# Performance work log

Measured on AMD Instinct MI355X. Metric: run time of the kernel, lower is better.

The kernel has to match this reference:

```python
import jax, jax.numpy as jnp
import numpy as np

N_NODES = 100000
IN_CH = 256
OUT_CH = 128
HEADS = 1
N_EDGES = 1600000
NEG_SLOPE = 0.2
EPS = 1e-16


def setup_inputs() -> dict:
    key = jax.random.key(0)
    ks = jax.random.split(key, 6)
    x = jax.random.normal(ks[0], (N_NODES, IN_CH), dtype=jnp.float32)
    edge_index = jax.random.randint(ks[1], (2, N_EDGES), 0, N_NODES, dtype=jnp.int64)
    # xavier-ish scaled params
    lin_src = jax.random.normal(ks[2], (IN_CH, OUT_CH), dtype=jnp.float32) * (1.414 * (2.0 / (IN_CH + OUT_CH)) ** 0.5)
    att_src = jax.random.normal(ks[3], (1, HEADS, OUT_CH), dtype=jnp.float32) * 0.1
    att_dst = jax.random.normal(ks[4], (1, HEADS, OUT_CH), dtype=jnp.float32) * 0.1
    bias = jnp.zeros((HEADS * OUT_CH,), dtype=jnp.float32)
    return {"x": x, "edge_index": edge_index, "lin_src": lin_src,
            "att_src": att_src, "att_dst": att_dst, "bias": bias}


def reference(x, edge_index, lin_src, att_src, att_dst, bias):
    N = x.shape[0]
    # shared projection (lin_dst is lin_src when in_channels is an int)
    xp = (x @ lin_src).reshape(N, HEADS, OUT_CH)  # [N, H, C]

    # add_self_loops: drop existing self-edges (via mask) and append N loop edges
    src, dst = edge_index[0], edge_index[1]
    loop = jnp.arange(N, dtype=edge_index.dtype)
    src_all = jnp.concatenate([src, loop])
    dst_all = jnp.concatenate([dst, loop])
    valid = jnp.concatenate([src != dst, jnp.ones((N,), dtype=bool)])  # [E+N]

    # per-node attention logits
    alpha_src = jnp.sum(xp * att_src, axis=-1)  # [N, H]
    alpha_dst = jnp.sum(xp * att_dst, axis=-1)  # [N, H]
    alpha = alpha_src[src_all] + alpha_dst[dst_all]  # [E+N, H]
    alpha = jax.nn.leaky_relu(alpha, NEG_SLOPE)

    # scatter softmax over incoming edges of each dst node (global-max stabilized,
    # matching the original src.max() over all retained edges)
    amax = jnp.max(jnp.where(valid[:, None], alpha, -jnp.inf))
    ex = jnp.exp(alpha - amax) * valid[:, None].astype(alpha.dtype)
    denom = jax.ops.segment_sum(ex, dst_all, num_segments=N)  # [N, H]
    alpha = ex / (denom[dst_all] + EPS)  # [E+N, H]

    # weighted aggregation
    weighted = xp[src_all] * alpha[..., None]  # [E+N, H, C]
    out = jax.ops.segment_sum(weighted, dst_all, num_segments=N)  # [N, H, C]

    out = out.reshape(N, HEADS * OUT_CH) + bias  # concat=True
    return out
```

## Files before the change

kernel.cpp:

```cpp
#include <hip/hip_runtime.h>
#include <cstdint>
#include <cstddef>

#define IN_CH 256
#define OUT_CH 128
#define NEG_SLOPE 0.2f
#define EPS 1e-16f

#define BM 64
#define BN 128
#define BK 32

__device__ __forceinline__ void gemm_body(
    int bid,
    const float* __restrict__ x, const float* __restrict__ w,
    const float* __restrict__ att_s, const float* __restrict__ att_d,
    float* __restrict__ xp, float* __restrict__ asrc, float* __restrict__ adst,
    int M)
{
    __shared__ float sA[BK][BM + 4];
    __shared__ float sB[BK][BN];
    const int tid = threadIdx.x;
    const int ty = tid >> 4;
    const int tx = tid & 15;
    const int row0 = bid * BM;

    float acc[4][8];
#pragma unroll
    for (int i = 0; i < 4; ++i)
#pragma unroll
        for (int j = 0; j < 8; ++j) acc[i][j] = 0.f;

    const int ar = tid >> 2;
    const int ak = (tid & 3) * 8;
    const int bk = tid >> 3;
    const int bn = (tid & 7) * 16;

    for (int k0 = 0; k0 < IN_CH; k0 += BK) {
        float4 va0 = make_float4(0.f, 0.f, 0.f, 0.f), va1 = va0;
        const int grow = row0 + ar;
        if (grow < M) {
            const float4* pa = (const float4*)(x + (size_t)grow * IN_CH + k0 + ak);
            va0 = pa[0]; va1 = pa[1];
        }
        sA[ak + 0][ar] = va0.x; sA[ak + 1][ar] = va0.y;
        sA[ak + 2][ar] = va0.z; sA[ak + 3][ar] = va0.w;
        sA[ak + 4][ar] = va1.x; sA[ak + 5][ar] = va1.y;
        sA[ak + 6][ar] = va1.z; sA[ak + 7][ar] = va1.w;

        {
            const float4* pb = (const float4*)(w + (size_t)(k0 + bk) * OUT_CH + bn);
            float4 vb0 = pb[0], vb1 = pb[1], vb2 = pb[2], vb3 = pb[3];
            float4* qb = (float4*)&sB[bk][bn];
            qb[0] = vb0; qb[1] = vb1; qb[2] = vb2; qb[3] = vb3;
        }
        __syncthreads();

#pragma unroll
        for (int k = 0; k < BK; ++k) {
            float4 a4 = *(const float4*)&sA[k][ty * 4];
            float4 b0 = *(const float4*)&sB[k][tx * 8];
            float4 b1 = *(const float4*)&sB[k][tx * 8 + 4];
            float a[4] = { a4.x, a4.y, a4.z, a4.w };
            float b[8] = { b0.x, b0.y, b0.z, b0.w, b1.x, b1.y, b1.z, b1.w };
#pragma unroll
            for (int i = 0; i < 4; ++i)
#pragma unroll
                for (int j = 0; j < 8; ++j)
                    acc[i][j] += a[i] * b[j];
        }
        __syncthreads();
    }

    float as[8], ad[8];
#pragma unroll
    for (int j = 0; j < 8; ++j) {
        as[j] = att_s[tx * 8 + j];
        ad[j] = att_d[tx * 8 + j];
    }
#pragma unroll
    for (int i = 0; i < 4; ++i) {
        const int r = row0 + ty * 4 + i;
        if (r < M) {
            float4 o0 = make_float4(acc[i][0], acc[i][1], acc[i][2], acc[i][3]);
            float4 o1 = make_float4(acc[i][4], acc[i][5], acc[i][6], acc[i][7]);
            float4* q = (float4*)(xp + (size_t)r * OUT_CH + tx * 8);
            q[0] = o0; q[1] = o1;
            float ps = 0.f, pd = 0.f;
#pragma unroll
            for (int j = 0; j < 8; ++j) {
                ps += acc[i][j] * as[j];
                pd += acc[i][j] * ad[j];
            }
#pragma unroll
            for (int m = 8; m >= 1; m >>= 1) {
                ps += __shfl_xor(ps, m, 16);
                pd += __shfl_xor(pd, m, 16);
            }
            if (tx == 0) { asrc[r] = ps; adst[r] = pd; }
        }
    }
}

__device__ __forceinline__ void hist_body(
    int bid, int nblk,
    const int* __restrict__ src, const int* __restrict__ dst,
    int* __restrict__ deg, int* __restrict__ pw, int E)
{
    const int T = nblk * 256;
    const int e0 = bid * 256 + threadIdx.x;
#pragma unroll
    for (int k = 0; k < 4; ++k) {
        const int e = e0 + k * T;
        if (e < E) {
            int s = src[e], d = dst[e];
            if (s != d) pw[e] = atomicAdd(&deg[d], 1);
        }
    }
}

__global__ __launch_bounds__(256) void fused_gemm_hist_kernel(
    const float* __restrict__ x, const float* __restrict__ w,
    const float* __restrict__ att_s, const float* __restrict__ att_d,
    float* __restrict__ xp, float* __restrict__ asrc, float* __restrict__ adst,
    int M,
    const int* __restrict__ src, const int* __restrict__ dst,
    int* __restrict__ deg, int* __restrict__ pw, int E,
    int gemm_blocks, int hist_blocks)
{
    if ((int)blockIdx.x < gemm_blocks) {
        gemm_body(blockIdx.x, x, w, att_s, att_d, xp, asrc, adst, M);
    } else {
        hist_body(blockIdx.x - gemm_blocks, hist_blocks, src, dst, deg, pw, E);
    }
}

#define SCAN_NB 256
#define SCAN_NT 256

__global__ __launch_bounds__(SCAN_NT) void scan_partial_kernel(
    const int* __restrict__ deg, int* __restrict__ bsum, int N)
{
    __shared__ int sh[SCAN_NT];
    const int chunk = (N + SCAN_NB - 1) / SCAN_NB;
    const int sub   = (chunk + SCAN_NT - 1) / SCAN_NT;
    const int b0 = blockIdx.x * chunk;
    const int t0 = b0 + threadIdx.x * sub;
    const int t1 = min(min(b0 + chunk, t0 + sub), N);
    int s = 0;
    for (int i = t0; i < t1; ++i) s += deg[i];
    sh[threadIdx.x] = s;
    __syncthreads();
    for (int off = SCAN_NT / 2; off > 0; off >>= 1) {
        if (threadIdx.x < off) sh[threadIdx.x] += sh[threadIdx.x + off];
        __syncthreads();
    }
    if (threadIdx.x == 0) bsum[blockIdx.x] = sh[0];
}

__global__ __launch_bounds__(SCAN_NB) void scan_blocksums_kernel(
    const int* __restrict__ bsum, int* __restrict__ boff,
    int* __restrict__ row_ptr, int N)
{
    __shared__ int sh[SCAN_NB];
    const int t = threadIdx.x;
    sh[t] = bsum[t];
    __syncthreads();
    for (int off = 1; off < SCAN_NB; off <<= 1) {
        int v = (t >= off) ? sh[t - off] : 0;
        __syncthreads();
        sh[t] += v;
        __syncthreads();
    }
    boff[t] = (t == 0) ? 0 : sh[t - 1];
    if (t == SCAN_NB - 1) row_ptr[N] = sh[t];
}

__global__ __launch_bounds__(SCAN_NT) void scan_fill_kernel(
    const int* __restrict__ deg, const int* __restrict__ boff,
    int* __restrict__ row_ptr, int N)
{
    __shared__ int sh[SCAN_NT];
    const int chunk = (N + SCAN_NB - 1) / SCAN_NB;
    const int sub   = (chunk + SCAN_NT - 1) / SCAN_NT;
    const int b0 = blockIdx.x * chunk;
    const int t0 = b0 + threadIdx.x * sub;
    const int t1 = min(min(b0 + chunk, t0 + sub), N);
    int s = 0;
    for (int i = t0; i < t1; ++i) s += deg[i];
    sh[threadIdx.x] = s;
    __syncthreads();
    for (int off = 1; off < SCAN_NT; off <<= 1) {
        int v = (threadIdx.x >= off) ? sh[threadIdx.x - off] : 0;
        __syncthreads();
        sh[threadIdx.x] += v;
        __syncthreads();
    }
    int run = boff[blockIdx.x] + ((threadIdx.x == 0) ? 0 : sh[threadIdx.x - 1]);
    for (int i = t0; i < t1; ++i) {
        row_ptr[i] = run;
        run += deg[i];
    }
}

__global__ __launch_bounds__(256) void scatter_kernel(
    const int* __restrict__ src, const int* __restrict__ dst,
    const int* __restrict__ row_ptr, const int* __restrict__ pw,
    int* __restrict__ col, int E, int nblk)
{
    const int T = nblk * 256;
    const int e0 = blockIdx.x * 256 + threadIdx.x;
#pragma unroll
    for (int k = 0; k < 4; ++k) {
        const int e = e0 + k * T;
        if (e < E) {
            int s = src[e], d = dst[e];
            if (s != d) col[row_ptr[d] + pw[e]] = s;
        }
    }
}

__global__ __launch_bounds__(256) void aggregate_kernel(
    const float* __restrict__ xp, const float* __restrict__ asrc,
    const float* __restrict__ adst, const int* __restrict__ row_ptr,
    const int* __restrict__ col, const float* __restrict__ bias,
    float* __restrict__ out, int N)
{
    const int wave = (blockIdx.x * blockDim.x + threadIdx.x) >> 6;
    const int lane = threadIdx.x & 63;
    if (wave >= N) return;
    const int n = wave;
    const float a_d = adst[n];

    const float2* xp2 = (const float2*)xp;
    float accx = 0.f, accy = 0.f, denom = 0.f;

    {
        float lg = asrc[n] + a_d;
        lg = (lg > 0.f) ? lg : lg * NEG_SLOPE;
        float ex = __expf(lg);
        denom += ex;
        float2 v = xp2[(size_t)n * 64 + lane];
        accx += ex * v.x; accy += ex * v.y;
    }

    const int beg = row_ptr[n];
    const int end = row_ptr[n + 1];
    for (int base = beg; base < end; base += 64) {
        const int idx = base + lane;
        int s = 0; float ex = 0.f;
        if (idx < end) {
            s = col[idx];
            float lg = asrc[s] + a_d;
            lg = (lg > 0.f) ? lg : lg * NEG_SLOPE;
            ex = __expf(lg);
        }
        const int cnt = min(64, end - base);
        for (int j = 0; j < cnt; ++j) {
            const float exj = __shfl(ex, j, 64);
            const int   sj  = __shfl(s, j, 64);
            denom += exj;
            float2 v = xp2[(size_t)sj * 64 + lane];
            accx += exj * v.x; accy += exj * v.y;
        }
    }

    const float inv = 1.f / (denom + EPS);
    const float2* bias2 = (const float2*)bias;
    float2 bv = bias2[lane];
    float2 o; o.x = accx * inv + bv.x; o.y = accy * inv + bv.y;
    ((float2*)out)[(size_t)n * 64 + lane] = o;
}

extern "C" void kernel_launch(void* const* d_in, const int* in_sizes, int n_in,
                              void* d_out, int out_size, void* d_ws, size_t ws_size,
                              hipStream_t stream)
{
    const float* x     = (const float*)d_in[0];
    const int*   ei    = (const int*)d_in[1];
    const float* w     = (const float*)d_in[2];
    const float* att_s = (const float*)d_in[3];
    const float* att_d = (const float*)d_in[4];
    const float* bias  = (const float*)d_in[5];
    float* out = (float*)d_out;

    const int N = in_sizes[0] / IN_CH;
    const int E = in_sizes[1] / 2;
    const int* src = ei;
    const int* dst = ei + E;

    char* p = (char*)d_ws;
    float* xp      = (float*)p; p += (size_t)N * OUT_CH * sizeof(float);
    float* asrc    = (float*)p; p += (size_t)N * sizeof(float);
    float* adst    = (float*)p; p += (size_t)N * sizeof(float);
    int*   deg     = (int*)p;   p += (size_t)N * sizeof(int);
    int*   row_ptr = (int*)p;   p += (size_t)(N + 1) * sizeof(int);
    int*   bsum    = (int*)p;   p += (size_t)SCAN_NB * sizeof(int);
    int*   boff    = (int*)p;   p += (size_t)SCAN_NB * sizeof(int);
    int*   pw      = (int*)p;   p += (size_t)E * sizeof(int);
    int*   col     = (int*)p;   p += (size_t)E * sizeof(int);

    hipMemsetAsync(deg, 0, (size_t)N * sizeof(int), stream);

    const int gemm_blocks = (N + BM - 1) / BM;
    const int hist_blocks = (E + 256 * 4 - 1) / (256 * 4);
    fused_gemm_hist_kernel<<<gemm_blocks + hist_blocks, 256, 0, stream>>>(
        x, w, att_s, att_d, xp, asrc, adst, N,
        src, dst, deg, pw, E, gemm_blocks, hist_blocks);

    scan_partial_kernel<<<SCAN_NB, SCAN_NT, 0, stream>>>(deg, bsum, N);
    scan_blocksums_kernel<<<1, SCAN_NB, 0, stream>>>(bsum, boff, row_ptr, N);
    scan_fill_kernel<<<SCAN_NB, SCAN_NT, 0, stream>>>(deg, boff, row_ptr, N);

    const int sc_blocks = (E + 256 * 4 - 1) / (256 * 4);
    scatter_kernel<<<sc_blocks, 256, 0, stream>>>(src, dst, row_ptr, pw, col, E, sc_blocks);

    aggregate_kernel<<<(N + 3) / 4, 256, 0, stream>>>(
        xp, asrc, adst, row_ptr, col, bias, out, N);
}
```

Before: 436.9 us.

## Use bf16 MFMA projection, store bf16 features, unroll aggregation gather

Replaces the FP32 SIMT GEMM with bf16 MFMA 16x16x32 instructions, using a pre-transposed bf16 copy of the weights made by a new conversion kernel. The projected features are stored as bf16, which halves the bytes read in the random gather of the aggregation kernel. The aggregation loop is unrolled by four with independent accumulators so more gather loads are in flight at once. Histogram and scatter kernels process eight edges per thread, and hist blocks are ordered before GEMM blocks. Reduced precision in the features and attention logits may loosen accuracy against the reference.

```diff
diff --git a/kernel.cpp b/kernel.cpp
--- a/kernel.cpp
+++ b/kernel.cpp
@@ -7,97 +7,85 @@
 #define NEG_SLOPE 0.2f
 #define EPS 1e-16f
 
-#define BM 64
-#define BN 128
-#define BK 32
+typedef __attribute__((ext_vector_type(8))) short bf16x8;
+typedef __attribute__((ext_vector_type(4))) float f32x4;
+
+__device__ __forceinline__ unsigned short f2bf(float f) {
+    unsigned int u = __float_as_uint(f);
+    return (unsigned short)((u + 0x7fffu + ((u >> 16) & 1u)) >> 16);
+}
+
+__global__ __launch_bounds__(256) void convert_w_kernel(const float* __restrict__ w,
+                                                        unsigned short* __restrict__ wt)
+{
+    const int n = blockIdx.x;
+    const int k = threadIdx.x;
+    wt[(size_t)n * IN_CH + k] = f2bf(w[(size_t)k * OUT_CH + n]);
+}
 
 __device__ __forceinline__ void gemm_body(
-    int bid,
-    const float* __restrict__ x, const float* __restrict__ w,
+    int bid, const float* __restrict__ x, const unsigned short* __restrict__ wt,
     const float* __restrict__ att_s, const float* __restrict__ att_d,
-    float* __restrict__ xp, float* __restrict__ asrc, float* __restrict__ adst,
+    unsigned short* __restrict__ xpb, float* __restrict__ asrc, float* __restrict__ adst,
     int M)
 {
-    __shared__ float sA[BK][BM + 4];
-    __shared__ float sB[BK][BN];
-    const int tid = threadIdx.x;
-    const int ty = tid >> 4;
-    const int tx = tid & 15;
-    const int row0 = bid * BM;
-
-    float acc[4][8];
-#pragma unroll
-    for (int i = 0; i < 4; ++i)
-#pragma unroll
-        for (int j = 0; j < 8; ++j) acc[i][j] = 0.f;
-
-    const int ar = tid >> 2;
-    const int ak = (tid & 3) * 8;
-    const int bk = tid >> 3;
-    const int bn = (tid & 7) * 16;
-
-    for (int k0 = 0; k0 < IN_CH; k0 += BK) {
-        float4 va0 = make_float4(0.f, 0.f, 0.f, 0.f), va1 = va0;
-        const int grow = row0 + ar;
-        if (grow < M) {
-            const float4* pa = (const float4*)(x + (size_t)grow * IN_CH + k0 + ak);
-            va0 = pa[0]; va1 = pa[1];
-        }
-        sA[ak + 0][ar] = va0.x; sA[ak + 1][ar] = va0.y;
-        sA[ak + 2][ar] = va0.z; sA[ak + 3][ar] = va0.w;
-        sA[ak + 4][ar] = va1.x; sA[ak + 5][ar] = va1.y;
-        sA[ak + 6][ar] = va1.z; sA[ak + 7][ar] = va1.w;
-
-        {
-            const float4* pb = (const float4*)(w + (size_t)(k0 + bk) * OUT_CH + bn);
-            float4 vb0 = pb[0], vb1 = pb[1], vb2 = pb[2], vb3 = pb[3];
-            float4* qb = (float4*)&sB[bk][bn];
-            qb[0] = vb0; qb[1] = vb1; qb[2] = vb2; qb[3] = vb3;
-        }
-        __syncthreads();
-
-#pragma unroll
-        for (int k = 0; k < BK; ++k) {
-            float4 a4 = *(const float4*)&sA[k][ty * 4];
-            float4 b0 = *(const float4*)&sB[k][tx * 8];
-            float4 b1 = *(const float4*)&sB[k][tx * 8 + 4];
-            float a[4] = { a4.x, a4.y, a4.z, a4.w };
-            float b[8] = { b0.x, b0.y, b0.z, b0.w, b1.x, b1.y, b1.z, b1.w };
-#pragma unroll
-            for (int i = 0; i < 4; ++i)
-#pragma unroll
-                for (int j = 0; j < 8; ++j)
-                    acc[i][j] += a[i] * b[j];
-        }
-        __syncthreads();
-    }
-
-    float as[8], ad[8];
-#pragma unroll
-    for (int j = 0; j < 8; ++j) {
-        as[j] = att_s[tx * 8 + j];
-        ad[j] = att_d[tx * 8 + j];
-    }
-#pragma unroll
-    for (int i = 0; i < 4; ++i) {
-        const int r = row0 + ty * 4 + i;
-        if (r < M) {
-            float4 o0 = make_float4(acc[i][0], acc[i][1], acc[i][2], acc[i][3]);
-            float4 o1 = make_float4(acc[i][4], acc[i][5], acc[i][6], acc[i][7]);
-            float4* q = (float4*)(xp + (size_t)r * OUT_CH + tx * 8);
-            q[0] = o0; q[1] = o1;
+    const int tid  = threadIdx.x;
+    const int wv   = tid >> 6;
+    const int lane = tid & 63;
+    const int lm   = lane & 15;
+    const int quad = lane >> 4;
+    const int arow = bid * 64 + wv * 16 + lm;
+    const bool av  = arow < M;
+    const float* xrow = x + (size_t)arow * IN_CH + quad * 8;
+
+    f32x4 acc[8];
+#pragma unroll
+    for (int t = 0; t < 8; ++t) acc[t] = (f32x4){0.f, 0.f, 0.f, 0.f};
+
+#pragma unroll
+    for (int kk = 0; kk < 8; ++kk) {
+        const int k0 = kk * 32;
+        bf16x8 af = {0, 0, 0, 0, 0, 0, 0, 0};
+        if (av) {
+            float4 a0 = *(const float4*)(xrow + k0);
+            float4 a1 = *(const float4*)(xrow + k0 + 4);
+            af[0] = (short)f2bf(a0.x); af[1] = (short)f2bf(a0.y);
+            af[2] = (short)f2bf(a0.z); af[3] = (short)f2bf(a0.w);
+            af[4] = (short)f2bf(a1.x); af[5] = (short)f2bf(a1.y);
+            af[6] = (short)f2bf(a1.z); af[7] = (short)f2bf(a1.w);
+        }
+#pragma unroll
+        for (int t = 0; t < 8; ++t) {
+            bf16x8 bf = *(const bf16x8*)(wt + (size_t)(16 * t + lm) * IN_CH + k0 + quad * 8);
+            acc[t] = __builtin_amdgcn_mfma_f32_16x16x32_bf16(af, bf, acc[t], 0, 0, 0);
+        }
+    }
+
+    float asw[8], adw[8];
+#pragma unroll
+    for (int t = 0; t < 8; ++t) {
+        asw[t] = att_s[16 * t + lm];
+        adw[t] = att_d[16 * t + lm];
+    }
+#pragma unroll
+    for (int r = 0; r < 4; ++r) {
+        const int orow = bid * 64 + wv * 16 + quad * 4 + r;
+        if (orow < M) {
             float ps = 0.f, pd = 0.f;
-#pragma unroll
-            for (int j = 0; j < 8; ++j) {
-                ps += acc[i][j] * as[j];
-                pd += acc[i][j] * ad[j];
+            unsigned short* xr = xpb + (size_t)orow * OUT_CH + lm;
+#pragma unroll
+            for (int t = 0; t < 8; ++t) {
+                float v = acc[t][r];
+                xr[16 * t] = f2bf(v);
+                ps += v * asw[t];
+                pd += v * adw[t];
             }
 #pragma unroll
-            for (int m = 8; m >= 1; m >>= 1) {
+            for (int m = 1; m < 16; m <<= 1) {
                 ps += __shfl_xor(ps, m, 16);
                 pd += __shfl_xor(pd, m, 16);
             }
-            if (tx == 0) { asrc[r] = ps; adst[r] = pd; }
+            if (lm == 0) { asrc[orow] = ps; adst[orow] = pd; }
         }
     }
 }
@@ -110,7 +98,7 @@
     const int T = nblk * 256;
     const int e0 = bid * 256 + threadIdx.x;
 #pragma unroll
-    for (int k = 0; k < 4; ++k) {
+    for (int k = 0; k < 8; ++k) {
         const int e = e0 + k * T;
         if (e < E) {
             int s = src[e], d = dst[e];
@@ -120,19 +108,18 @@
 }
 
 __global__ __launch_bounds__(256) void fused_gemm_hist_kernel(
-    const float* __restrict__ x, const float* __restrict__ w,
+    const float* __restrict__ x, const unsigned short* __restrict__ wt,
     const float* __restrict__ att_s, const float* __restrict__ att_d,
-    float* __restrict__ xp, float* __restrict__ asrc, float* __restrict__ adst,
+    unsigned short* __restrict__ xpb, float* __restrict__ asrc, float* __restrict__ adst,
     int M,
     const int* __restrict__ src, const int* __restrict__ dst,
     int* __restrict__ deg, int* __restrict__ pw, int E,
-    int gemm_blocks, int hist_blocks)
-{
-    if ((int)blockIdx.x < gemm_blocks) {
-        gemm_body(blockIdx.x, x, w, att_s, att_d, xp, asrc, adst, M);
-    } else {
-        hist_body(blockIdx.x - gemm_blocks, hist_blocks, src, dst, deg, pw, E);
-    }
+    int hist_blocks)
+{
+    if ((int)blockIdx.x < hist_blocks)
+        hist_body(blockIdx.x, hist_blocks, src, dst, deg, pw, E);
+    else
+        gemm_body(blockIdx.x - hist_blocks, x, wt, att_s, att_d, xpb, asrc, adst, M);
 }
 
 #define SCAN_NB 256
@@ -211,7 +198,7 @@
     const int T = nblk * 256;
     const int e0 = blockIdx.x * 256 + threadIdx.x;
 #pragma unroll
-    for (int k = 0; k < 4; ++k) {
+    for (int k = 0; k < 8; ++k) {
         const int e = e0 + k * T;
         if (e < E) {
             int s = src[e], d = dst[e];
@@ -221,31 +208,32 @@
 }
 
 __global__ __launch_bounds__(256) void aggregate_kernel(
-    const float* __restrict__ xp, const float* __restrict__ asrc,
+    const unsigned short* __restrict__ xpb, const float* __restrict__ asrc,
     const float* __restrict__ adst, const int* __restrict__ row_ptr,
     const int* __restrict__ col, const float* __restrict__ bias,
     float* __restrict__ out, int N)
 {
-    const int wave = (blockIdx.x * blockDim.x + threadIdx.x) >> 6;
+    const int n = (int)((blockIdx.x * blockDim.x + threadIdx.x) >> 6);
     const int lane = threadIdx.x & 63;
-    if (wave >= N) return;
-    const int n = wave;
+    if (n >= N) return;
     const float a_d = adst[n];
-
-    const float2* xp2 = (const float2*)xp;
-    float accx = 0.f, accy = 0.f, denom = 0.f;
+    const unsigned int* xpw = (const unsigned int*)xpb;
+
+    float ax0 = 0.f, ay0 = 0.f, ax1 = 0.f, ay1 = 0.f;
+    float ax2 = 0.f, ay2 = 0.f, ax3 = 0.f, ay3 = 0.f;
+    float den = 0.f;
 
     {
         float lg = asrc[n] + a_d;
         lg = (lg > 0.f) ? lg : lg * NEG_SLOPE;
         float ex = __expf(lg);
-        denom += ex;
-        float2 v = xp2[(size_t)n * 64 + lane];
-        accx += ex * v.x; accy += ex * v.y;
-    }
-
-    const int beg = row_ptr[n];
-    const int end = row_ptr[n + 1];
+        den += ex;
+        unsigned int v = xpw[(size_t)n * 64 + lane];
+        ax0 += ex * __uint_as_float(v << 16);
+        ay0 += ex * __uint_as_float(v & 0xffff0000u);
+    }
+
+    const int beg = row_ptr[n], end = row_ptr[n + 1];
     for (int base = beg; base < end; base += 64) {
         const int idx = base + lane;
         int s = 0; float ex = 0.f;
@@ -256,19 +244,41 @@
             ex = __expf(lg);
         }
         const int cnt = min(64, end - base);
-        for (int j = 0; j < cnt; ++j) {
-            const float exj = __shfl(ex, j, 64);
-            const int   sj  = __shfl(s, j, 64);
-            denom += exj;
-            float2 v = xp2[(size_t)sj * 64 + lane];
-            accx += exj * v.x; accy += exj * v.y;
-        }
-    }
-
-    const float inv = 1.f / (denom + EPS);
-    const float2* bias2 = (const float2*)bias;
-    float2 bv = bias2[lane];
-    float2 o; o.x = accx * inv + bv.x; o.y = accy * inv + bv.y;
+        int j = 0;
+        for (; j + 4 <= cnt; j += 4) {
+            float e0 = __shfl(ex, j, 64),     e1 = __shfl(ex, j + 1, 64);
+            float e2 = __shfl(ex, j + 2, 64), e3 = __shfl(ex, j + 3, 64);
+            int   s0 = __shfl(s, j, 64),      s1 = __shfl(s, j + 1, 64);
+            int   s2 = __shfl(s, j + 2, 64),  s3 = __shfl(s, j + 3, 64);
+            unsigned int v0 = xpw[(size_t)s0 * 64 + lane];
+            unsigned int v1 = xpw[(size_t)s1 * 64 + lane];
+            unsigned int v2 = xpw[(size_t)s2 * 64 + lane];
+            unsigned int v3 = xpw[(size_t)s3 * 64 + lane];
+            den += (e0 + e1) + (e2 + e3);
+            ax0 += e0 * __uint_as_float(v0 << 16);
+            ay0 += e0 * __uint_as_float(v0 & 0xffff0000u);
+            ax1 += e1 * __uint_as_float(v1 << 16);
+            ay1 += e1 * __uint_as_float(v1 & 0xffff0000u);
+            ax2 += e2 * __uint_as_float(v2 << 16);
+            ay2 += e2 * __uint_as_float(v2 & 0xffff0000u);
+            ax3 += e3 * __uint_as_float(v3 << 16);
+            ay3 += e3 * __uint_as_float(v3 & 0xffff0000u);
+        }
+        for (; j < cnt; ++j) {
+            float e0 = __shfl(ex, j, 64);
+            int   s0 = __shfl(s, j, 64);
+            unsigned int v0 = xpw[(size_t)s0 * 64 + lane];
+            den += e0;
+            ax0 += e0 * __uint_as_float(v0 << 16);
+            ay0 += e0 * __uint_as_float(v0 & 0xffff0000u);
+        }
+    }
+
+    const float inv = 1.f / (den + EPS);
+    const float2 bv = ((const float2*)bias)[lane];
+    float2 o;
+    o.x = ((ax0 + ax1) + (ax2 + ax3)) * inv + bv.x;
+    o.y = ((ay0 + ay1) + (ay2 + ay3)) * inv + bv.y;
     ((float2*)out)[(size_t)n * 64 + lane] = o;
 }
 
@@ -290,31 +300,34 @@
     const int* dst = ei + E;
 
     char* p = (char*)d_ws;
-    float* xp      = (float*)p; p += (size_t)N * OUT_CH * sizeof(float);
-    float* asrc    = (float*)p; p += (size_t)N * sizeof(float);
-    float* adst    = (float*)p; p += (size_t)N * sizeof(float);
-    int*   deg     = (int*)p;   p += (size_t)N * sizeof(int);
-    int*   row_ptr = (int*)p;   p += (size_t)(N + 1) * sizeof(int);
-    int*   bsum    = (int*)p;   p += (size_t)SCAN_NB * sizeof(int);
-    int*   boff    = (int*)p;   p += (size_t)SCAN_NB * sizeof(int);
-    int*   pw      = (int*)p;   p += (size_t)E * sizeof(int);
-    int*   col     = (int*)p;   p += (size_t)E * sizeof(int);
-
-    hipMemsetAsync(deg, 0, (size_t)N * sizeof(int), stream);
-
-    const int gemm_blocks = (N + BM - 1) / BM;
-    const int hist_blocks = (E + 256 * 4 - 1) / (256 * 4);
-    fused_gemm_hist_kernel<<<gemm_blocks + hist_blocks, 256, 0, stream>>>(
-        x, w, att_s, att_d, xp, asrc, adst, N,
-        src, dst, deg, pw, E, gemm_blocks, hist_blocks);
+    auto take = [&](size_t bytes) { char* q = p; p += (bytes + 255) & ~size_t(255); return q; };
+    unsigned short* xpb = (unsigned short*)take((size_t)N * OUT_CH * 2);
+    unsigned short* wt  = (unsigned short*)take((size_t)OUT_CH * IN_CH * 2);
+    float* asrc   = (float*)take((size_t)N * 4);
+    float* adst   = (float*)take((size_t)N * 4);
+    int*   deg    = (int*)take((size_t)N * 4);
+    int*   row_ptr= (int*)take((size_t)(N + 1) * 4);
+    int*   bsum   = (int*)take(SCAN_NB * 4);
+    int*   boff   = (int*)take(SCAN_NB * 4);
+    int*   pw     = (int*)take((size_t)E * 4);
+    int*   col    = (int*)take((size_t)E * 4);
+
+    hipMemsetAsync(deg, 0, (size_t)N * 4, stream);
+    convert_w_kernel<<<OUT_CH, IN_CH, 0, stream>>>(w, wt);
+
+    const int gemm_blocks = (N + 63) / 64;
+    const int hist_blocks = (E + 256 * 8 - 1) / (256 * 8);
+    fused_gemm_hist_kernel<<<hist_blocks + gemm_blocks, 256, 0, stream>>>(
+        x, wt, att_s, att_d, xpb, asrc, adst, N,
+        src, dst, deg, pw, E, hist_blocks);
 
     scan_partial_kernel<<<SCAN_NB, SCAN_NT, 0, stream>>>(deg, bsum, N);
     scan_blocksums_kernel<<<1, SCAN_NB, 0, stream>>>(bsum, boff, row_ptr, N);
     scan_fill_kernel<<<SCAN_NB, SCAN_NT, 0, stream>>>(deg, boff, row_ptr, N);
 
-    const int sc_blocks = (E + 256 * 4 - 1) / (256 * 4);
+    const int sc_blocks = (E + 256 * 8 - 1) / (256 * 8);
     scatter_kernel<<<sc_blocks, 256, 0, stream>>>(src, dst, row_ptr, pw, col, E, sc_blocks);
 
     aggregate_kernel<<<(N + 3) / 4, 256, 0, stream>>>(
-        xp, asrc, adst, row_ptr, col, bias, out, N);
-}
+        xpb, asrc, adst, row_ptr, col, bias, out, N);
+}
```

New measurement: 381.2 us. -12.7%, faster.
